# Optimization experiments

Hardware: AMD Instinct MI355X
Metric: run time of the kernel (lower is better)

## Reference

```python
import jax, jax.numpy as jnp
import numpy as np

B, S, D, H = 2, 2048, 1024, 16
HD = D // H

def setup_inputs() -> dict:
    key = jax.random.key(0)
    ks = jax.random.split(key, 9)
    s = 1.0 / np.sqrt(D)
    inp = {"x": jax.random.normal(ks[0], (B, S, D), dtype=jnp.float32)}
    for i, name in enumerate(["q", "k", "v", "o"]):
        inp[f"W_{name}"] = jax.random.uniform(ks[1 + 2 * i], (D, D), dtype=jnp.float32, minval=-s, maxval=s)
        inp[f"b_{name}"] = jax.random.uniform(ks[2 + 2 * i], (D,), dtype=jnp.float32, minval=-s, maxval=s)
    return inp


def reference(x, W_q, b_q, W_k, b_k, W_v, b_v, W_o, b_o):
    # x: [B, S, D]
    def split_heads(t):
        return t.reshape(B, S, H, HD).transpose(0, 2, 1, 3)  # [B, H, S, HD]

    Q = split_heads(x @ W_q + b_q)
    K = split_heads(x @ W_k + b_k)
    V = split_heads(x @ W_v + b_v)

    scale = 1.0 / np.sqrt(HD).astype(np.float32)
    scores = jnp.einsum("bhqd,bhkd->bhqk", Q, K) * scale  # [B, H, S, S]
    weights = jax.nn.softmax(scores, axis=-1)
    attn = jnp.einsum("bhqk,bhkd->bhqd", weights, V)  # [B, H, S, HD]
    attn = attn.transpose(0, 2, 1, 3).reshape(B, S, D)
    return attn @ W_o + b_o
```

## Files before the change

kernel.cpp:

```cpp
#include <hip/hip_runtime.h>
#include <hip/hip_bf16.h>

#define BB 2
#define SS 2048
#define DD 1024
#define HH 16
#define HD 64

typedef __attribute__((ext_vector_type(8))) short bf16x8;
typedef __attribute__((ext_vector_type(4))) float f32x4;

__device__ __forceinline__ unsigned short f2bf(float f) {
  unsigned int u = __float_as_uint(f);
  return (unsigned short)((u + 0x7FFFu + ((u >> 16) & 1u)) >> 16);
}

__device__ __forceinline__ float fast_exp2(float x) {
#if __has_builtin(__builtin_amdgcn_exp2f)
  return __builtin_amdgcn_exp2f(x);
#else
  return __expf(x * 0.6931471805599453f);
#endif
}

__device__ __forceinline__ void async_copy16(const unsigned short* gp, unsigned short* lp) {
  __builtin_amdgcn_global_load_lds(
      (const __attribute__((address_space(1))) unsigned int*)gp,
      (__attribute__((address_space(3))) unsigned int*)lp, 16, 0, 0);
}

__device__ __forceinline__ void pl32_swap(unsigned& a, unsigned& b) {
#if __has_builtin(__builtin_amdgcn_permlane32_swap)
  auto r = __builtin_amdgcn_permlane32_swap(a, b, false, false);
  a = r[0];
  b = r[1];
#else
  asm volatile("v_permlane32_swap_b32 %0, %1" : "+v"(a), "+v"(b));
#endif
}
__device__ __forceinline__ void pl16_swap(unsigned& a, unsigned& b) {
#if __has_builtin(__builtin_amdgcn_permlane16_swap)
  auto r = __builtin_amdgcn_permlane16_swap(a, b, false, false);
  a = r[0];
  b = r[1];
#else
  asm volatile("v_permlane16_swap_b32 %0, %1" : "+v"(a), "+v"(b));
#endif
}

__global__ __launch_bounds__(256) void prep_kernel(
    const float* __restrict__ x, unsigned short* __restrict__ xb,
    const float* __restrict__ W0, unsigned short* __restrict__ T0,
    const float* __restrict__ W1, unsigned short* __restrict__ T1,
    const float* __restrict__ W2, unsigned short* __restrict__ T2,
    const float* __restrict__ W3, unsigned short* __restrict__ T3) {
  const int blk = blockIdx.x;
  const int t = threadIdx.x;
  if (blk < 4096) {
    int i = blk * 1024 + t * 4;
    float4 v = *(const float4*)(x + i);
    ushort4 u;
    u.x = f2bf(v.x); u.y = f2bf(v.y); u.z = f2bf(v.z); u.w = f2bf(v.w);
    *(ushort4*)(xb + i) = u;
    return;
  }
  const int j = blk - 4096;
  const int jw = j >> 10;
  const int tb = j & 1023;
  const float* W = jw == 0 ? W0 : (jw == 1 ? W1 : (jw == 2 ? W2 : W3));
  unsigned short* T = jw == 0 ? T0 : (jw == 1 ? T1 : (jw == 2 ? T2 : T3));
  __shared__ float tile[32][33];
  int k0 = (tb & 31) * 32, n0 = (tb >> 5) * 32;
  int c = t & 31, r0 = t >> 5;
#pragma unroll
  for (int i = 0; i < 4; ++i) {
    int r = r0 + i * 8;
    tile[r][c] = W[(size_t)(k0 + r) * DD + n0 + c];
  }
  __syncthreads();
#pragma unroll
  for (int i = 0; i < 4; ++i) {
    int r = r0 + i * 8;
    T[(size_t)(n0 + r) * DD + k0 + c] = f2bf(tile[c][r]);
  }
}

__global__ __launch_bounds__(256, 3) void out_gemm_tri(
    const unsigned short* __restrict__ A, const unsigned short* __restrict__ BT,
    const float* __restrict__ bias, float* __restrict__ out) {
  const int i = blockIdx.x;
  const int xcd = i & 7;
  const int slot = i >> 3;
  const int bm = (xcd + 8 * (slot >> 3)) * 128;
  const int bn = (slot & 7) * 128;

  const int t = threadIdx.x;
  const int w = t >> 6;
  const int l = t & 63;
  const int wm = (w >> 1) * 64;
  const int wn = (w & 1) * 64;
  const int fr = l & 15;
  const int kgB = (l >> 4) * 16;

  __shared__ __align__(16) unsigned short lds[2][3][4096];

  f32x4 acc[4][4];
#pragma unroll
  for (int ii = 0; ii < 4; ++ii)
#pragma unroll
    for (int j = 0; j < 4; ++j) acc[ii][j] = (f32x4)0.f;

  int aoff[4], boff[4];
#pragma unroll
  for (int ii = 0; ii < 4; ++ii) {
    aoff[ii] = (wm + ii * 16 + fr) * 64 + kgB;
    boff[ii] = (wn + ii * 16 + fr) * 64 + kgB;
  }

  const int cc0 = w * 128 + l;
  const int cc1 = cc0 + 64;
  const int row0 = cc0 >> 2, kk0 = (cc0 & 3) * 8;
  const int row1 = cc1 >> 2, kk1 = (cc1 & 3) * 8;
  const unsigned short* a0 = A + (size_t)(bm + row0) * DD + kk0;
  const unsigned short* a1 = A + (size_t)(bm + row1) * DD + kk1;
  const unsigned short* b0 = BT + (size_t)(bn + row0) * DD + kk0;
  const unsigned short* b1 = BT + (size_t)(bn + row1) * DD + kk1;

  auto stage_tile = [&](int T) {
    if (T >= 32) return;
    const int buf = T % 3;
    const int k0 = T * 32;
    async_copy16(a0 + k0, &lds[0][buf][w * 1024]);
    async_copy16(a1 + k0, &lds[0][buf][w * 1024 + 512]);
    async_copy16(b0 + k0, &lds[1][buf][w * 1024]);
    async_copy16(b1 + k0, &lds[1][buf][w * 1024 + 512]);
  };

  auto phase = [&](int T, int vm) {
    const int buf = T % 3;
    const char* Ab = (const char*)&lds[0][buf][0];
    const char* Bb = (const char*)&lds[1][buf][0];
    bf16x8 af[4], bfr[4];
#pragma unroll
    for (int ii = 0; ii < 4; ++ii) af[ii] = *(const bf16x8*)(Ab + aoff[ii]);
#pragma unroll
    for (int j = 0; j < 4; ++j) bfr[j] = *(const bf16x8*)(Bb + boff[j]);
    stage_tile(T + 2);
    asm volatile("s_barrier" ::: "memory");
    __builtin_amdgcn_s_setprio(1);
#pragma unroll
    for (int ii = 0; ii < 4; ++ii)
#pragma unroll
      for (int j = 0; j < 4; ++j)
        acc[ii][j] = __builtin_amdgcn_mfma_f32_16x16x32_bf16(af[ii], bfr[j], acc[ii][j], 0, 0, 0);
    __builtin_amdgcn_s_setprio(0);
    if (vm == 1) asm volatile("s_waitcnt vmcnt(4)" ::: "memory");
    if (vm == 2) asm volatile("s_waitcnt vmcnt(0)" ::: "memory");
    asm volatile("s_barrier" ::: "memory");
  };

  stage_tile(0);
  stage_tile(1);
  asm volatile("s_waitcnt vmcnt(4)" ::: "memory");
  asm volatile("s_barrier" ::: "memory");

  for (int T = 0; T < 30; ++T) phase(T, 1);
  phase(30, 2);
  phase(31, 0);

  const int col_l = l & 15;
  const int row_l = (l >> 4) * 4;

#pragma unroll
  for (int ii = 0; ii < 4; ++ii) {
    int m_base = bm + wm + ii * 16 + row_l;
#pragma unroll
    for (int j = 0; j < 4; ++j) {
      int n = bn + wn + j * 16 + col_l;
      float bv = bias[n];
#pragma unroll
      for (int r = 0; r < 4; ++r)
        out[(size_t)(m_base + r) * DD + n] = acc[ii][j][r] + bv;
    }
  }
}

__global__ __launch_bounds__(256, 3) void qkv_gemm_tri(
    const unsigned short* __restrict__ A,
    const unsigned short* __restrict__ WqT, const unsigned short* __restrict__ WkT,
    const unsigned short* __restrict__ WvT,
    const float* __restrict__ bq, const float* __restrict__ bk,
    const float* __restrict__ bv,
    unsigned short* __restrict__ Qo, unsigned short* __restrict__ Ko,
    unsigned short* __restrict__ VTo) {
  const int i = blockIdx.x;
  const int xcd = i & 7;
  const int slot = i >> 3;
  const int bm = (xcd + 8 * (slot / 24)) * 128;
  const int c = slot % 24;
  const int which = c >> 3;
  const int bn = (c & 7) * 128;
  const unsigned short* BT = which == 0 ? WqT : (which == 1 ? WkT : WvT);
  const float* bias = which == 0 ? bq : (which == 1 ? bk : bv);

  const int t = threadIdx.x;
  const int w = t >> 6;
  const int l = t & 63;
  const int wm = (w >> 1) * 64;
  const int wn = (w & 1) * 64;
  const int fr = l & 15;
  const int kgB = (l >> 4) * 16;

  __shared__ __align__(16) unsigned short lds[2][3][4096];

  f32x4 acc[4][4];
#pragma unroll
  for (int ii = 0; ii < 4; ++ii)
#pragma unroll
    for (int j = 0; j < 4; ++j) acc[ii][j] = (f32x4)0.f;

  int aoff[4], boff[4];
#pragma unroll
  for (int ii = 0; ii < 4; ++ii) {
    aoff[ii] = (wm + ii * 16 + fr) * 64 + kgB;
    boff[ii] = (wn + ii * 16 + fr) * 64 + kgB;
  }

  const int cc0 = w * 128 + l;
  const int cc1 = cc0 + 64;
  const int row0 = cc0 >> 2, kk0 = (cc0 & 3) * 8;
  const int row1 = cc1 >> 2, kk1 = (cc1 & 3) * 8;
  const unsigned short* a0 = A + (size_t)(bm + row0) * DD + kk0;
  const unsigned short* a1 = A + (size_t)(bm + row1) * DD + kk1;
  const unsigned short* b0 = BT + (size_t)(bn + row0) * DD + kk0;
  const unsigned short* b1 = BT + (size_t)(bn + row1) * DD + kk1;

  auto stage_tile = [&](int T) {
    if (T >= 32) return;
    const int buf = T % 3;
    const int k0 = T * 32;
    async_copy16(a0 + k0, &lds[0][buf][w * 1024]);
    async_copy16(a1 + k0, &lds[0][buf][w * 1024 + 512]);
    async_copy16(b0 + k0, &lds[1][buf][w * 1024]);
    async_copy16(b1 + k0, &lds[1][buf][w * 1024 + 512]);
  };

  auto phase = [&](int T, int vm) {
    const int buf = T % 3;
    const char* Ab = (const char*)&lds[0][buf][0];
    const char* Bb = (const char*)&lds[1][buf][0];
    bf16x8 af[4], bfr[4];
#pragma unroll
    for (int ii = 0; ii < 4; ++ii) af[ii] = *(const bf16x8*)(Ab + aoff[ii]);
#pragma unroll
    for (int j = 0; j < 4; ++j) bfr[j] = *(const bf16x8*)(Bb + boff[j]);
    stage_tile(T + 2);
    asm volatile("s_barrier" ::: "memory");
    __builtin_amdgcn_s_setprio(1);
#pragma unroll
    for (int ii = 0; ii < 4; ++ii)
#pragma unroll
      for (int j = 0; j < 4; ++j)
        acc[ii][j] = __builtin_amdgcn_mfma_f32_16x16x32_bf16(af[ii], bfr[j], acc[ii][j], 0, 0, 0);
    __builtin_amdgcn_s_setprio(0);
    if (vm == 1) asm volatile("s_waitcnt vmcnt(4)" ::: "memory");
    if (vm == 2) asm volatile("s_waitcnt vmcnt(0)" ::: "memory");
    asm volatile("s_barrier" ::: "memory");
  };

  stage_tile(0);
  stage_tile(1);
  asm volatile("s_waitcnt vmcnt(4)" ::: "memory");
  asm volatile("s_barrier" ::: "memory");

  for (int T = 0; T < 30; ++T) phase(T, 1);
  phase(30, 2);
  phase(31, 0);

  const int col_l = l & 15;
  const int row_l = (l >> 4) * 4;
  const int b_ = bm >> 11;

  if (which != 2) {
    const float scl = which == 0 ? 0.18033688011112042f : 1.0f;
    unsigned short* out = which == 0 ? Qo : Ko;
#pragma unroll
    for (int ii = 0; ii < 4; ++ii) {
      int m_base = bm + wm + ii * 16 + row_l;
#pragma unroll
      for (int j = 0; j < 4; ++j) {
        int n = bn + wn + j * 16 + col_l;
        float bv = bias[n];
        int h_ = n >> 6, hd_ = n & 63;
#pragma unroll
        for (int r = 0; r < 4; ++r) {
          int m = m_base + r;
          int b2 = m >> 11, s_ = m & 2047;
          out[(((size_t)(b2 * HH + h_) * SS) + s_) * HD + hd_] =
              f2bf((acc[ii][j][r] + bv) * scl);
        }
      }
    }
  } else {
    unsigned short* out = VTo;
    unsigned int* Tt = (unsigned int*)&lds[0][0][0];
    const int srow0 = bm & 2047;
#pragma unroll
    for (int p = 0; p < 4; ++p) {
      __syncthreads();
      if ((w & 1) == (p >> 1)) {
        const int jt0 = (p & 1) * 2;
#pragma unroll
        for (int jj = 0; jj < 2; ++jj) {
          int jt = jt0 + jj;
          int n_p = jj * 16 + col_l;
          float bv = bias[bn + p * 32 + n_p];
#pragma unroll
          for (int ii = 0; ii < 4; ++ii) {
            int m0 = wm + ii * 16 + row_l;
#pragma unroll
            for (int pr = 0; pr < 2; ++pr) {
              unsigned int val =
                  (unsigned int)f2bf(acc[ii][jt][2 * pr] + bv) |
                  ((unsigned int)f2bf(acc[ii][jt][2 * pr + 1] + bv) << 16);
              int m = m0 + 2 * pr;
              Tt[n_p * 64 + (((m >> 1)) ^ ((n_p & 7) << 2))] = val;
            }
          }
        }
      }
      __syncthreads();
#pragma unroll
      for (int cq = 0; cq < 2; ++cq) {
        int q = t + cq * 256;
        int n_p = q >> 4, cpos = q & 15;
        uint4 v = *(const uint4*)(Tt + n_p * 64 + ((cpos * 4) ^ ((n_p & 7) << 2)));
        int n_glob = bn + p * 32 + n_p;
        int h_ = n_glob >> 6, hd_ = n_glob & 63;
        *(uint4*)(out + ((size_t)((b_ * HH + h_) * HD + hd_)) * SS + srow0 + cpos * 8) = v;
      }
    }
  }
}

__global__ __launch_bounds__(512, 2) void flash_attn_mfma(
    const unsigned short* __restrict__ Q,
    const unsigned short* __restrict__ K,
    const unsigned short* __restrict__ VT,
    unsigned short* __restrict__ ctx) {
  const int bh = blockIdx.x;
  const int qt = blockIdx.y;
  const int b  = bh >> 4;
  const int h  = bh & 15;
  const int t  = threadIdx.x;
  const int w  = t >> 6;
  const int l  = t & 63;
  const int wg = w & 3;
  const int wh = w >> 2;
  const int g  = l >> 4;
  const int ln = l & 15;

  const unsigned short* Qp = Q + ((size_t)bh * SS + (size_t)qt * 128 + wg * 32) * HD;
  const unsigned short* Kp = K + (size_t)bh * SS * HD;
  const unsigned short* Vp = VT + (size_t)bh * HD * SS;

  __shared__ __align__(16) unsigned short smem[2][2][3][2048];
  __shared__ __align__(16) float rred[4 * 64 * 2];

  bf16x8 qf[2][2];
#pragma unroll
  for (int nt = 0; nt < 2; ++nt)
#pragma unroll
    for (int kb = 0; kb < 2; ++kb)
      qf[nt][kb] = *(const bf16x8*)(Qp + (nt * 16 + ln) * HD + kb * 32 + g * 8);

  f32x4 o[2][4];
#pragma unroll
  for (int nt = 0; nt < 2; ++nt)
#pragma unroll
    for (int mt = 0; mt < 4; ++mt) o[nt][mt] = (f32x4)0.f;
  float rs[2] = {0.f, 0.f};

  const int sp  = w >> 2;
  const int sq  = w & 3;
  const int idx = sq * 64 + l;
  const int rowK = idx >> 3;
  const int gccK = (idx & 7) ^ (rowK & 7);
  const unsigned short* kgp = Kp + (size_t)(sp * 32 + rowK) * HD + gccK * 8;
  const int rowV = idx >> 2;
  const int gc2V = (idx & 3) ^ ((rowV >> 1) & 3);
  const unsigned short* vgp = Vp + (size_t)rowV * SS + sp * 32 + gc2V * 8;
  unsigned short* dK = &smem[0][sp][0][sq * 512];
  unsigned short* dV = &smem[1][sp][0][sq * 512];

  int ko[2][2];
#pragma unroll
  for (int kb = 0; kb < 2; ++kb)
#pragma unroll
    for (int mt = 0; mt < 2; ++mt) {
      int row = mt * 16 + ln;
      ko[kb][mt] = row * 128 + (((kb * 4 + g) ^ (row & 7)) * 16);
    }
  int vo[4];
#pragma unroll
  for (int mt = 0; mt < 4; ++mt) {
    int row = mt * 16 + ln;
    vo[mt] = row * 64 + ((g ^ ((row >> 1) & 3)) * 16);
  }
  const char* kpar = (const char*)&smem[0][wh][0][0];
  const char* vpar = (const char*)&smem[1][wh][0][0];

  auto stage_i = [&](int buf) {
    async_copy16(kgp, dK + buf * 2048);
    async_copy16(vgp, dV + buf * 2048);
    kgp += 64 * HD;
    vgp += 64;
  };

  auto phase = [&](int buf, int sbuf, bool doStage, int vm) {
    const char* Kst = kpar + buf * 4096;
    const char* Vst = vpar + buf * 4096;

    bf16x8 ka[2][2], va[4];
#pragma unroll
    for (int kb = 0; kb < 2; ++kb)
#pragma unroll
      for (int mt = 0; mt < 2; ++mt)
        ka[kb][mt] = *(const bf16x8*)(Kst + ko[kb][mt]);
#pragma unroll
    for (int mt = 0; mt < 4; ++mt) va[mt] = *(const bf16x8*)(Vst + vo[mt]);

    if (doStage) stage_i(sbuf);
    asm volatile("s_barrier" ::: "memory");
    __builtin_amdgcn_s_setprio(1);

    f32x4 st[2][2];
#pragma unroll
    for (int nt = 0; nt < 2; ++nt)
#pragma unroll
      for (int mt = 0; mt < 2; ++mt) st[nt][mt] = (f32x4)0.f;
#pragma unroll
    for (int kb = 0; kb < 2; ++kb)
#pragma unroll
      for (int mt = 0; mt < 2; ++mt) {
        st[0][mt] = __builtin_amdgcn_mfma_f32_16x16x32_bf16(ka[kb][mt], qf[0][kb], st[0][mt], 0, 0, 0);
        st[1][mt] = __builtin_amdgcn_mfma_f32_16x16x32_bf16(ka[kb][mt], qf[1][kb], st[1][mt], 0, 0, 0);
      }

    unsigned Sd[2][2][2];
#pragma unroll
    for (int nt = 0; nt < 2; ++nt) {
#pragma unroll
      for (int mt = 0; mt < 2; ++mt) {
        float p0 = fast_exp2(st[nt][mt][0]);
        float p1 = fast_exp2(st[nt][mt][1]);
        float p2 = fast_exp2(st[nt][mt][2]);
        float p3 = fast_exp2(st[nt][mt][3]);
        Sd[nt][mt][0] = __builtin_amdgcn_perm(__float_as_uint(p1), __float_as_uint(p0),
                                              0x07060302u);
        Sd[nt][mt][1] = __builtin_amdgcn_perm(__float_as_uint(p3), __float_as_uint(p2),
                                              0x07060302u);
        rs[nt] += (p0 + p1) + (p2 + p3);
      }
#pragma unroll
      for (int p = 0; p < 2; ++p) pl32_swap(Sd[nt][0][p], Sd[nt][1][p]);
#pragma unroll
      for (int p = 0; p < 2; ++p) pl16_swap(Sd[nt][0][p], Sd[nt][1][p]);
    }

    bf16x8 pbv[2];
#pragma unroll
    for (int nt = 0; nt < 2; ++nt) {
      union { unsigned u[4]; bf16x8 v; } cu;
      cu.u[0] = Sd[nt][0][0];
      cu.u[1] = Sd[nt][0][1];
      cu.u[2] = Sd[nt][1][0];
      cu.u[3] = Sd[nt][1][1];
      pbv[nt] = cu.v;
    }
#pragma unroll
    for (int mt = 0; mt < 4; ++mt) {
      o[0][mt] = __builtin_amdgcn_mfma_f32_16x16x32_bf16(va[mt], pbv[0], o[0][mt], 0, 0, 0);
      o[1][mt] = __builtin_amdgcn_mfma_f32_16x16x32_bf16(va[mt], pbv[1], o[1][mt], 0, 0, 0);
    }

    __builtin_amdgcn_s_setprio(0);
    if (vm == 1) asm volatile("s_waitcnt vmcnt(2)" ::: "memory");
    if (vm == 2) asm volatile("s_waitcnt vmcnt(0)" ::: "memory");
    asm volatile("s_barrier" ::: "memory");
  };

  stage_i(0);
  stage_i(1);
  asm volatile("s_waitcnt vmcnt(2)" ::: "memory");
  asm volatile("s_barrier" ::: "memory");

  for (int it = 0; it < 10; ++it) {
    phase(0, 2, true, 1);
    phase(1, 0, true, 1);
    phase(2, 1, true, 1);
  }
  phase(0, 0, false, 2);
  phase(1, 0, false, 0);

  __syncthreads();
  {
    float* ored = (float*)&smem[0][0][0][0];
    float* rb = ored + (wg * 64 + l) * 32;
    float* sb = rred + (wg * 64 + l) * 2;
    if (wh == 1) {
#pragma unroll
      for (int nt = 0; nt < 2; ++nt)
#pragma unroll
        for (int mt = 0; mt < 4; ++mt) {
          int idx2 = nt * 4 + mt;
          *(f32x4*)(rb + ((unsigned)(idx2 ^ (l & 7)) * 4)) = o[nt][mt];
        }
      sb[0] = rs[0];
      sb[1] = rs[1];
    }
    __syncthreads();
    if (wh == 1) return;
#pragma unroll
    for (int nt = 0; nt < 2; ++nt)
#pragma unroll
      for (int mt = 0; mt < 4; ++mt) {
        int idx2 = nt * 4 + mt;
        f32x4 pv = *(const f32x4*)(rb + ((unsigned)(idx2 ^ (l & 7)) * 4));
        o[nt][mt] += pv;
      }
    rs[0] += sb[0];
    rs[1] += sb[1];
  }

#pragma unroll
  for (int nt = 0; nt < 2; ++nt) {
    float lsum = rs[nt];
    lsum += __shfl_xor(lsum, 16, 64);
    lsum += __shfl_xor(lsum, 32, 64);
    float inv = 1.f / lsum;
    int srow = qt * 128 + wg * 32 + nt * 16 + ln;
    unsigned short* cb = ctx + (size_t)(b * SS + srow) * DD + h * HD;
#pragma unroll
    for (int mt = 0; mt < 4; ++mt) {
      ushort4 u4;
      u4.x = f2bf(o[nt][mt][0] * inv);
      u4.y = f2bf(o[nt][mt][1] * inv);
      u4.z = f2bf(o[nt][mt][2] * inv);
      u4.w = f2bf(o[nt][mt][3] * inv);
      *(ushort4*)(cb + mt * 16 + 4 * g) = u4;
    }
  }
}

extern "C" void kernel_launch(void* const* d_in, const int* in_sizes, int n_in,
                              void* d_out, int out_size, void* d_ws, size_t ws_size,
                              hipStream_t stream) {
  const float* x  = (const float*)d_in[0];
  const float* Wq = (const float*)d_in[1];
  const float* bq = (const float*)d_in[2];
  const float* Wk = (const float*)d_in[3];
  const float* bk = (const float*)d_in[4];
  const float* Wv = (const float*)d_in[5];
  const float* bv = (const float*)d_in[6];
  const float* Wo = (const float*)d_in[7];
  const float* bo = (const float*)d_in[8];
  float* out = (float*)d_out;

  const size_t ELEMS = (size_t)BB * SS * DD;
  char* ws = (char*)d_ws;
  unsigned short* xb   = (unsigned short*)ws;  ws += ELEMS * 2;
  unsigned short* WqT  = (unsigned short*)ws;  ws += (size_t)DD * DD * 2;
  unsigned short* WkT  = (unsigned short*)ws;  ws += (size_t)DD * DD * 2;
  unsigned short* WvT  = (unsigned short*)ws;  ws += (size_t)DD * DD * 2;
  unsigned short* WoT  = (unsigned short*)ws;  ws += (size_t)DD * DD * 2;
  unsigned short* Qb   = (unsigned short*)ws;  ws += ELEMS * 2;
  unsigned short* Kb   = (unsigned short*)ws;  ws += ELEMS * 2;
  unsigned short* VbT  = (unsigned short*)ws;  ws += ELEMS * 2;
  unsigned short* ctxb = (unsigned short*)ws;  ws += ELEMS * 2;

  prep_kernel<<<8192, 256, 0, stream>>>(x, xb, Wq, WqT, Wk, WkT, Wv, WvT, Wo, WoT);

  qkv_gemm_tri<<<768, 256, 0, stream>>>(xb, WqT, WkT, WvT, bq, bk, bv,
                                        Qb, Kb, VbT);

  dim3 attn_grid(BB * HH, SS / 128);
  flash_attn_mfma<<<attn_grid, 512, 0, stream>>>(Qb, Kb, VbT, ctxb);

  out_gemm_tri<<<256, 256, 0, stream>>>(ctxb, WoT, bo, out);
}
```

Baseline: 179.9 us.

## Process two KV tiles per phase with software-pipelined softmax and double-pair buffering

The attention inner loop now handles two 64-key tiles per barrier phase. Each staging step brings in two tiles, and the LDS ring grows from 3 to 4 slots arranged as two pairs. Within a phase, the QK MFMA for tile B is interleaved with the softmax of tile A, and the PV MFMA for tile A is interleaved with the softmax of tile B, which halves the barriers and lets exp work overlap matrix work. The cost is more registers, more LDS, and a full vmcnt(0) wait at the end of each phase instead of a partial one, which can expose load latency.

```diff
diff --git a/kernel.cpp b/kernel.cpp
--- a/kernel.cpp
+++ b/kernel.cpp
@@ -364,7 +364,7 @@
   const unsigned short* Kp = K + (size_t)bh * SS * HD;
   const unsigned short* Vp = VT + (size_t)bh * HD * SS;
 
-  __shared__ __align__(16) unsigned short smem[2][2][3][2048];
+  __shared__ __align__(16) unsigned short smem[2][2][4][2048];
   __shared__ __align__(16) float rred[4 * 64 * 2];
 
   bf16x8 qf[2][2];
@@ -410,43 +410,16 @@
   const char* kpar = (const char*)&smem[0][wh][0][0];
   const char* vpar = (const char*)&smem[1][wh][0][0];
 
-  auto stage_i = [&](int buf) {
-    async_copy16(kgp, dK + buf * 2048);
-    async_copy16(vgp, dV + buf * 2048);
-    kgp += 64 * HD;
-    vgp += 64;
+  auto stage2 = [&](int b0_, int b1_) {
+    async_copy16(kgp, dK + b0_ * 2048);
+    async_copy16(kgp + 64 * HD, dK + b1_ * 2048);
+    async_copy16(vgp, dV + b0_ * 2048);
+    async_copy16(vgp + 64, dV + b1_ * 2048);
+    kgp += 128 * HD;
+    vgp += 128;
   };
 
-  auto phase = [&](int buf, int sbuf, bool doStage, int vm) {
-    const char* Kst = kpar + buf * 4096;
-    const char* Vst = vpar + buf * 4096;
-
-    bf16x8 ka[2][2], va[4];
-#pragma unroll
-    for (int kb = 0; kb < 2; ++kb)
-#pragma unroll
-      for (int mt = 0; mt < 2; ++mt)
-        ka[kb][mt] = *(const bf16x8*)(Kst + ko[kb][mt]);
-#pragma unroll
-    for (int mt = 0; mt < 4; ++mt) va[mt] = *(const bf16x8*)(Vst + vo[mt]);
-
-    if (doStage) stage_i(sbuf);
-    asm volatile("s_barrier" ::: "memory");
-    __builtin_amdgcn_s_setprio(1);
-
-    f32x4 st[2][2];
-#pragma unroll
-    for (int nt = 0; nt < 2; ++nt)
-#pragma unroll
-      for (int mt = 0; mt < 2; ++mt) st[nt][mt] = (f32x4)0.f;
-#pragma unroll
-    for (int kb = 0; kb < 2; ++kb)
-#pragma unroll
-      for (int mt = 0; mt < 2; ++mt) {
-        st[0][mt] = __builtin_amdgcn_mfma_f32_16x16x32_bf16(ka[kb][mt], qf[0][kb], st[0][mt], 0, 0, 0);
-        st[1][mt] = __builtin_amdgcn_mfma_f32_16x16x32_bf16(ka[kb][mt], qf[1][kb], st[1][mt], 0, 0, 0);
-      }
-
+  auto softmax = [&](f32x4 st[2][2], bf16x8 pbv[2]) {
     unsigned Sd[2][2][2];
 #pragma unroll
     for (int nt = 0; nt < 2; ++nt) {
@@ -466,11 +439,6 @@
       for (int p = 0; p < 2; ++p) pl32_swap(Sd[nt][0][p], Sd[nt][1][p]);
 #pragma unroll
       for (int p = 0; p < 2; ++p) pl16_swap(Sd[nt][0][p], Sd[nt][1][p]);
-    }
-
-    bf16x8 pbv[2];
-#pragma unroll
-    for (int nt = 0; nt < 2; ++nt) {
       union { unsigned u[4]; bf16x8 v; } cu;
       cu.u[0] = Sd[nt][0][0];
       cu.u[1] = Sd[nt][0][1];
@@ -478,30 +446,95 @@
       cu.u[3] = Sd[nt][1][1];
       pbv[nt] = cu.v;
     }
+  };
+
+  auto phase = [&](int ba, int bb, int sa, int sb, bool doStage, bool doVm) {
+    const char* KA = kpar + ba * 4096;
+    const char* VA = vpar + ba * 4096;
+
+    bf16x8 kaA[2][2], vaA[4];
+#pragma unroll
+    for (int kb = 0; kb < 2; ++kb)
+#pragma unroll
+      for (int mt = 0; mt < 2; ++mt)
+        kaA[kb][mt] = *(const bf16x8*)(KA + ko[kb][mt]);
+#pragma unroll
+    for (int mt = 0; mt < 4; ++mt) vaA[mt] = *(const bf16x8*)(VA + vo[mt]);
+
+    if (doStage) stage2(sa, sb);
+    asm volatile("s_barrier" ::: "memory");
+    __builtin_amdgcn_s_setprio(1);
+
+    f32x4 stA[2][2];
+#pragma unroll
+    for (int nt = 0; nt < 2; ++nt)
+#pragma unroll
+      for (int mt = 0; mt < 2; ++mt) stA[nt][mt] = (f32x4)0.f;
+#pragma unroll
+    for (int kb = 0; kb < 2; ++kb)
+#pragma unroll
+      for (int mt = 0; mt < 2; ++mt) {
+        stA[0][mt] = __builtin_amdgcn_mfma_f32_16x16x32_bf16(kaA[kb][mt], qf[0][kb], stA[0][mt], 0, 0, 0);
+        stA[1][mt] = __builtin_amdgcn_mfma_f32_16x16x32_bf16(kaA[kb][mt], qf[1][kb], stA[1][mt], 0, 0, 0);
+      }
+
+    const char* KB = kpar + bb * 4096;
+    const char* VB = vpar + bb * 4096;
+    bf16x8 kaB[2][2], vaB[4];
+#pragma unroll
+    for (int kb = 0; kb < 2; ++kb)
+#pragma unroll
+      for (int mt = 0; mt < 2; ++mt)
+        kaB[kb][mt] = *(const bf16x8*)(KB + ko[kb][mt]);
+#pragma unroll
+    for (int mt = 0; mt < 4; ++mt) vaB[mt] = *(const bf16x8*)(VB + vo[mt]);
+
+    bf16x8 pbvA[2];
+    softmax(stA, pbvA);
+
+    f32x4 stB[2][2];
+#pragma unroll
+    for (int nt = 0; nt < 2; ++nt)
+#pragma unroll
+      for (int mt = 0; mt < 2; ++mt) stB[nt][mt] = (f32x4)0.f;
+#pragma unroll
+    for (int kb = 0; kb < 2; ++kb)
+#pragma unroll
+      for (int mt = 0; mt < 2; ++mt) {
+        stB[0][mt] = __builtin_amdgcn_mfma_f32_16x16x32_bf16(kaB[kb][mt], qf[0][kb], stB[0][mt], 0, 0, 0);
+        stB[1][mt] = __builtin_amdgcn_mfma_f32_16x16x32_bf16(kaB[kb][mt], qf[1][kb], stB[1][mt], 0, 0, 0);
+      }
+
 #pragma unroll
     for (int mt = 0; mt < 4; ++mt) {
-      o[0][mt] = __builtin_amdgcn_mfma_f32_16x16x32_bf16(va[mt], pbv[0], o[0][mt], 0, 0, 0);
-      o[1][mt] = __builtin_amdgcn_mfma_f32_16x16x32_bf16(va[mt], pbv[1], o[1][mt], 0, 0, 0);
+      o[0][mt] = __builtin_amdgcn_mfma_f32_16x16x32_bf16(vaA[mt], pbvA[0], o[0][mt], 0, 0, 0);
+      o[1][mt] = __builtin_amdgcn_mfma_f32_16x16x32_bf16(vaA[mt], pbvA[1], o[1][mt], 0, 0, 0);
+    }
+
+    bf16x8 pbvB[2];
+    softmax(stB, pbvB);
+
+#pragma unroll
+    for (int mt = 0; mt < 4; ++mt) {
+      o[0][mt] = __builtin_amdgcn_mfma_f32_16x16x32_bf16(vaB[mt], pbvB[0], o[0][mt], 0, 0, 0);
+      o[1][mt] = __builtin_amdgcn_mfma_f32_16x16x32_bf16(vaB[mt], pbvB[1], o[1][mt], 0, 0, 0);
     }
 
     __builtin_amdgcn_s_setprio(0);
-    if (vm == 1) asm volatile("s_waitcnt vmcnt(2)" ::: "memory");
-    if (vm == 2) asm volatile("s_waitcnt vmcnt(0)" ::: "memory");
+    if (doVm) asm volatile("s_waitcnt vmcnt(0)" ::: "memory");
     asm volatile("s_barrier" ::: "memory");
   };
 
-  stage_i(0);
-  stage_i(1);
-  asm volatile("s_waitcnt vmcnt(2)" ::: "memory");
+  stage2(0, 1);
+  asm volatile("s_waitcnt vmcnt(0)" ::: "memory");
   asm volatile("s_barrier" ::: "memory");
 
-  for (int it = 0; it < 10; ++it) {
-    phase(0, 2, true, 1);
-    phase(1, 0, true, 1);
-    phase(2, 1, true, 1);
-  }
-  phase(0, 0, false, 2);
-  phase(1, 0, false, 0);
+  for (int it = 0; it < 7; ++it) {
+    phase(0, 1, 2, 3, true, true);
+    phase(2, 3, 0, 1, true, true);
+  }
+  phase(0, 1, 2, 3, true, true);
+  phase(2, 3, 0, 1, false, false);
 
   __syncthreads();
   {
```

Measured after the change: 189.5 us. 1.05x slower.
